# Performance work log

Hardware: AMD Instinct MI355X
Metric: run time of the kernel (lower is better)

Reference implementation:

```python
import jax, jax.numpy as jnp
import numpy as np

B, T, C, H = 8, 1024, 768, 12
D = C // H  # head_dim = 64

def _rope_tables(seq_len, d, base=10000.0):
    inv_freq = 1.0 / (base ** (jnp.arange(0, d, 2, dtype=jnp.float32) / d))  # [d/2]
    freqs = jnp.outer(jnp.arange(seq_len, dtype=jnp.float32), inv_freq)      # [T, d/2]
    return jnp.cos(freqs), jnp.sin(freqs)

def _apply_rotary(x, cos, sin):
    # x: [B,T,H,D]; cos/sin: [1,T,1,D/2]
    d = x.shape[-1] // 2
    x1, x2 = x[..., :d], x[..., d:]
    return jnp.concatenate([x1 * cos + x2 * sin, -x1 * sin + x2 * cos], axis=-1)

def setup_inputs() -> dict:
    key = jax.random.key(0)
    k1, k2, k3 = jax.random.split(key, 3)
    x = jax.random.normal(k1, (B, T, C), dtype=jnp.float32)
    w_qkv = jax.random.normal(k2, (3 * C, C), dtype=jnp.float32) * (C ** -0.5)
    w_proj = jax.random.normal(k3, (C, C), dtype=jnp.float32) * (C ** -0.5)
    return {"x": x, "w_qkv": w_qkv, "w_proj": w_proj}

def reference(x, w_qkv, w_proj):
    Bb, Tt, Cc = x.shape
    qkv = x @ w_qkv.T                                   # [B,T,3C]
    q, k, v = jnp.split(qkv, 3, axis=2)
    q = q.reshape(Bb, Tt, H, D)
    k = k.reshape(Bb, Tt, H, D)
    v = v.reshape(Bb, Tt, H, D)
    cos, sin = _rope_tables(Tt, D)
    cos = cos[None, :, None, :]
    sin = sin[None, :, None, :]
    q = _apply_rotary(q, cos, sin)
    k = _apply_rotary(k, cos, sin)
    scale = 1.0 / jnp.sqrt(jnp.float32(D))
    scores = jnp.einsum('bthd,bshd->bhts', q, k) * scale  # [B,H,T,T]
    causal = jnp.tril(jnp.ones((Tt, Tt), dtype=bool))
    scores = jnp.where(causal[None, None], scores, jnp.finfo(scores.dtype).min)
    p = jax.nn.softmax(scores, axis=-1)
    y = jnp.einsum('bhts,bshd->bthd', p, v).reshape(Bb, Tt, Cc)
    return y @ w_proj.T
```

## Files before the change

### kernel.cpp

```cpp
#include <hip/hip_runtime.h>
#include <hip/hip_bf16.h>

#define Bb 8
#define Tt 1024
#define Cc 768
#define Hh 12
#define Dd 64
#define M_ROWS (Bb * Tt)
#define QKV_N (3 * Cc)

typedef __attribute__((ext_vector_type(8))) short s16x8;
typedef __attribute__((ext_vector_type(4))) short s16x4;
typedef __attribute__((ext_vector_type(4))) float f32x4;

#define AS1 __attribute__((address_space(1)))
#define AS3 __attribute__((address_space(3)))

static __device__ __forceinline__ short f2bf(float f) {
    union { float f; unsigned u; } v; v.f = f;
    unsigned r = (v.u + 0x7fffu + ((v.u >> 16) & 1u)) >> 16;
    return (short)r;
}
static __device__ __forceinline__ unsigned pkt(float hi, float lo) {
    union { float f; unsigned u; } a, b; a.f = hi; b.f = lo;
    return __builtin_amdgcn_perm(a.u, b.u, 0x07060302u);
}

static __device__ __forceinline__ void cast8(const float* __restrict__ in,
                                             short* __restrict__ out, int i) {
    const float4 a = ((const float4*)in)[i * 2];
    const float4 b = ((const float4*)in)[i * 2 + 1];
    s16x8 f;
    f[0] = f2bf(a.x); f[1] = f2bf(a.y); f[2] = f2bf(a.z); f[3] = f2bf(a.w);
    f[4] = f2bf(b.x); f[5] = f2bf(b.y); f[6] = f2bf(b.z); f[7] = f2bf(b.w);
    ((s16x8*)out)[i] = f;
}

#define S1 (M_ROWS * Cc / 8)
#define S2 (QKV_N * Cc / 8)
#define S3 (Cc * Cc / 8)
#define SROPE (Tt * 32)
#define PREP_THREADS (S1 + S2 + S3 + SROPE)

__global__ __launch_bounds__(256) void prep_kernel(const float* __restrict__ x,
                                                   const float* __restrict__ wqkv,
                                                   const float* __restrict__ wproj,
                                                   short* __restrict__ xb,
                                                   short* __restrict__ wqkvb,
                                                   short* __restrict__ wprojb,
                                                   float2* __restrict__ cs) {
    int idx = blockIdx.x * blockDim.x + threadIdx.x;
    if (idx < S1) { cast8(x, xb, idx); return; }
    idx -= S1;
    if (idx < S2) {
        int row = idx / 96;
        int c8  = idx - row * 96;
        int q2 = (row >> 4) & 3;
        int src = (row < 2 * Cc && (q2 == 1 || q2 == 2)) ? (row ^ 0x30) : row;
        const float4 a = ((const float4*)(wqkv + (size_t)src * Cc))[c8 * 2];
        const float4 b = ((const float4*)(wqkv + (size_t)src * Cc))[c8 * 2 + 1];
        s16x8 f;
        f[0] = f2bf(a.x); f[1] = f2bf(a.y); f[2] = f2bf(a.z); f[3] = f2bf(a.w);
        f[4] = f2bf(b.x); f[5] = f2bf(b.y); f[6] = f2bf(b.z); f[7] = f2bf(b.w);
        ((s16x8*)wqkvb)[idx] = f;
        return;
    }
    idx -= S2;
    if (idx < S3) { cast8(wproj, wprojb, idx); return; }
    idx -= S3;
    {
        int t = idx >> 5, i = idx & 31;
        float inv_freq = exp2f(-0.41524101186092037f * (float)i);
        float fr = (float)t * inv_freq;
        float2 v; v.x = cosf(fr); v.y = sinf(fr);
        cs[idx] = v;
    }
}

template <int MODE, int TN>
__global__ __launch_bounds__(256, 3) void gemm_nt_mfma(const short* __restrict__ A,
                                                       const short* __restrict__ B,
                                                       void* __restrict__ Cout,
                                                       const float2* __restrict__ cs,
                                                       int M, int N, int K, int nblocks) {
    __shared__ short As[2][128 * 32];
    __shared__ short Bs[2][TN * 32];
    constexpr int NTW = TN / 32;

    const int wave = threadIdx.x >> 6;
    const int lane = threadIdx.x & 63;
    const int l16  = lane & 15;
    const int quad = lane >> 4;
    const int wr = wave >> 1;
    const int wc = wave & 1;

    const int mb8  = (M >> 7) >> 3;
    const int xcd  = blockIdx.x & 7;
    const int slot = blockIdx.x >> 3;
    const int bm = (xcd * mb8 + slot / nblocks) * 128;
    const int bn = (slot % nblocks) * TN;

    f32x4 acc[4][NTW] = {};

    auto stage = [&](int k0, int buf) {
#pragma unroll
        for (int j = 0; j < 2; j++) {
            const int D = j * 256 + wave * 64 + lane;
            const int G = D >> 3;
            const int s = (G << 3) | ((D & 7) ^ (G & 7));
            const int m = s >> 2, c4 = (s & 3) * 8;
            __builtin_amdgcn_global_load_lds(
                (const AS1 unsigned*)(A + (size_t)(bm + m) * K + k0 + c4),
                (AS3 unsigned*)&As[buf][(j * 256 + wave * 64) * 8], 16, 0, 0);
        }
        constexpr int BCH = TN * 4;
#pragma unroll
        for (int j = 0; j < (BCH + 255) / 256; j++) {
            if (BCH % 256 == 0 || j * 256 + wave * 64 < BCH) {
                const int D = j * 256 + wave * 64 + lane;
                const int G = D >> 3;
                const int s = (G << 3) | ((D & 7) ^ (G & 7));
                const int m = s >> 2, c4 = (s & 3) * 8;
                __builtin_amdgcn_global_load_lds(
                    (const AS1 unsigned*)(B + (size_t)(bn + m) * K + k0 + c4),
                    (AS3 unsigned*)&Bs[buf][(j * 256 + wave * 64) * 8], 16, 0, 0);
            }
        }
    };

    const int nIter = K >> 5;
    stage(0, 0);
    for (int kt = 0; kt < nIter; kt++) {
        const int buf = kt & 1;
        __syncthreads();
        if (kt + 1 < nIter) stage((kt + 1) << 5, buf ^ 1);

        s16x8 af[4];
#pragma unroll
        for (int mt = 0; mt < 4; mt++) {
            const int m = wr * 64 + mt * 16 + l16;
            const int d = ((m & 1) * 4 + quad) ^ ((m >> 1) & 7);
            af[mt] = *(const s16x8*)&As[buf][(m >> 1) * 64 + d * 8];
        }
#pragma unroll
        for (int nt = 0; nt < NTW; nt++) {
            const int n = wc * (TN / 2) + nt * 16 + l16;
            const int d = ((n & 1) * 4 + quad) ^ ((n >> 1) & 7);
            s16x8 bf = *(const s16x8*)&Bs[buf][(n >> 1) * 64 + d * 8];
#pragma unroll
            for (int mt = 0; mt < 4; mt++)
                acc[mt][nt] = __builtin_amdgcn_mfma_f32_16x16x32_bf16(
                    af[mt], bf, acc[mt][nt], 0, 0, 0);
        }
    }

    if constexpr (MODE == 0) {
#pragma unroll
        for (int mt = 0; mt < 4; mt++)
#pragma unroll
            for (int r = 0; r < 4; r++) {
                const size_t row = bm + wr * 64 + mt * 16 + quad * 4 + r;
#pragma unroll
                for (int nt = 0; nt < NTW; nt++)
                    ((float*)Cout)[row * N + bn + wc * (TN / 2) + nt * 16 + l16] =
                        acc[mt][nt][r];
            }
    } else {
        const bool is_v = (bn >= 2 * Cc);
        if (is_v) {
#pragma unroll
            for (int mt = 0; mt < 4; mt++)
#pragma unroll
                for (int r = 0; r < 4; r++) {
                    const size_t row = bm + wr * 64 + mt * 16 + quad * 4 + r;
#pragma unroll
                    for (int nt = 0; nt < NTW; nt++)
                        ((short*)Cout)[row * N + bn + wc * (TN / 2) + nt * 16 + l16] =
                            f2bf(acc[mt][nt][r]);
                }
        } else {
            const float scale = (bn < Cc) ? 0.125f : 1.0f;
#pragma unroll
            for (int mt = 0; mt < 4; mt++) {
#pragma unroll
                for (int r = 0; r < 4; r++) {
                    const int row = bm + wr * 64 + mt * 16 + quad * 4 + r;
                    const int t = row & (Tt - 1);
                    short* cp = (short*)Cout + (size_t)row * N + bn + wc * (TN / 2);
#pragma unroll
                    for (int p = 0; p < NTW; p += 2) {
                        const int g = wc * NTW + p;
                        const int i0 = ((g & 2) ? 16 : 0) + l16;
                        const float2 c0 = cs[t * 32 + i0];
                        const float x1 = acc[mt][p][r];
                        const float x2 = acc[mt][p + 1][r];
                        cp[p * 16 + l16]        = f2bf((x1 * c0.x + x2 * c0.y) * scale);
                        cp[(p + 1) * 16 + l16]  = f2bf((-x1 * c0.y + x2 * c0.x) * scale);
                    }
                }
            }
        }
    }
}

#define KSP 72
#define VSP 72

__global__ __launch_bounds__(256, 3) void flash_attn(const short* __restrict__ qkv,
                                                     short* __restrict__ y) {
    __shared__ short Ks[2][64 * KSP];
    __shared__ short Vs[2][64 * VSP];

    const int wave = threadIdx.x >> 6;
    const int lane = threadIdx.x & 63;
    const int l16  = lane & 15;
    const int quad = lane >> 4;

    const int pair = blockIdx.x / 96;
    const int bh   = blockIdx.x % 96;
    const int h = bh % Hh;
    const int b = bh / Hh;
    const int qa_blk = pair;
    const int qb_blk = 15 - pair;
    const int q0a = qa_blk * 64 + wave * 16;
    const int q0b = qb_blk * 64 + wave * 16;

    s16x8 qfa[2], qfb[2];
    {
        const short* qpa = qkv + (size_t)(b * Tt + q0a + l16) * QKV_N + h * Dd + quad * 8;
        const short* qpb = qkv + (size_t)(b * Tt + q0b + l16) * QKV_N + h * Dd + quad * 8;
        qfa[0] = *(const s16x8*)qpa;  qfa[1] = *(const s16x8*)(qpa + 32);
        qfb[0] = *(const s16x8*)qpb;  qfb[1] = *(const s16x8*)(qpb + 32);
    }

    f32x4 oa[4] = {}, ob[4] = {};
    float la = 0.f, lb = 0.f;

    const int krow = threadIdx.x >> 2;
    const int kd0  = (threadIdx.x & 3) * 16;
    const int key2 = (threadIdx.x & 31) * 2;
    const int dv0  = (threadIdx.x >> 5) * 8;

    s16x8 pk0, pk1, pv0, pv1;
    auto load_tile = [&](int kbase) {
        const short* kp = qkv + (size_t)(b * Tt + kbase + krow) * QKV_N + Cc + h * Dd + kd0;
        pk0 = *(const s16x8*)kp;
        pk1 = *(const s16x8*)(kp + 8);
        const short* vp = qkv + (size_t)(b * Tt + kbase + key2) * QKV_N + 2 * Cc + h * Dd + dv0;
        pv0 = *(const s16x8*)vp;
        pv1 = *(const s16x8*)(vp + QKV_N);
    };
    auto store_tile = [&](int buf) {
        *(s16x8*)&Ks[buf][krow * KSP + kd0]     = pk0;
        *(s16x8*)&Ks[buf][krow * KSP + kd0 + 8] = pk1;
#pragma unroll
        for (int j = 0; j < 8; j++) {
            ushort2 w; w.x = (unsigned short)pv0[j]; w.y = (unsigned short)pv1[j];
            *(ushort2*)&Vs[buf][(dv0 + j) * VSP + key2] = w;
        }
    };

    auto process_pair = [&](int buf, int kbase, bool mask_a) {
        short* pwb = &Ks[buf ^ 1][wave * 16 * KSP];
        short* pwa = &Vs[buf ^ 1][wave * 16 * VSP];
        f32x4 eb[4], ea[4];
#pragma unroll
        for (int g = 0; g < 4; g++) {
            s16x8 kf0 = *(const s16x8*)&Ks[buf][(g * 16 + l16) * KSP + quad * 8];
            s16x8 kf1 = *(const s16x8*)&Ks[buf][(g * 16 + l16) * KSP + 32 + quad * 8];
            f32x4 zb = {}, za = {};
            zb = __builtin_amdgcn_mfma_f32_16x16x32_bf16(kf0, qfb[0], zb, 0, 0, 0);
            zb = __builtin_amdgcn_mfma_f32_16x16x32_bf16(kf1, qfb[1], zb, 0, 0, 0);
            za = __builtin_amdgcn_mfma_f32_16x16x32_bf16(kf0, qfa[0], za, 0, 0, 0);
            za = __builtin_amdgcn_mfma_f32_16x16x32_bf16(kf1, qfa[1], za, 0, 0, 0);
            eb[g] = zb; ea[g] = za;
        }
        float rsb = 0.f, rsa = 0.f;
#pragma unroll
        for (int g = 0; g < 4; g++) {
#pragma unroll
            for (int r = 0; r < 4; r++) {
                float pb = __expf(eb[g][r]); rsb += pb; eb[g][r] = pb;
                float pa = __expf(ea[g][r]);
                if (mask_a) pa = (kbase + g * 16 + quad * 4 + r <= q0a + l16) ? pa : 0.0f;
                rsa += pa; ea[g][r] = pa;
            }
            uint2 ub, ua;
            ub.x = pkt(eb[g][1], eb[g][0]); ub.y = pkt(eb[g][3], eb[g][2]);
            ua.x = pkt(ea[g][1], ea[g][0]); ua.y = pkt(ea[g][3], ea[g][2]);
            *(uint2*)&pwb[l16 * KSP + g * 16 + quad * 4] = ub;
            *(uint2*)&pwa[l16 * VSP + g * 16 + quad * 4] = ua;
        }
        lb += rsb; la += rsa;
#pragma unroll
        for (int c = 0; c < 2; c++) {
            s16x8 pbb = *(const s16x8*)&pwb[l16 * KSP + c * 32 + quad * 8];
            s16x8 pba = *(const s16x8*)&pwa[l16 * VSP + c * 32 + quad * 8];
#pragma unroll
            for (int nc = 0; nc < 4; nc++) {
                s16x8 vb = *(const s16x8*)&Vs[buf][(nc * 16 + l16) * VSP + c * 32 + quad * 8];
                ob[nc] = __builtin_amdgcn_mfma_f32_16x16x32_bf16(vb, pbb, ob[nc], 0, 0, 0);
                oa[nc] = __builtin_amdgcn_mfma_f32_16x16x32_bf16(vb, pba, oa[nc], 0, 0, 0);
            }
        }
    };

    auto process_single = [&](int buf, int kbase, bool masked) {
        short* pw = &Ks[buf ^ 1][wave * 16 * KSP];
        f32x4 e[4];
#pragma unroll
        for (int g = 0; g < 4; g++) {
            s16x8 kf0 = *(const s16x8*)&Ks[buf][(g * 16 + l16) * KSP + quad * 8];
            s16x8 kf1 = *(const s16x8*)&Ks[buf][(g * 16 + l16) * KSP + 32 + quad * 8];
            f32x4 z = {};
            z = __builtin_amdgcn_mfma_f32_16x16x32_bf16(kf0, qfb[0], z, 0, 0, 0);
            z = __builtin_amdgcn_mfma_f32_16x16x32_bf16(kf1, qfb[1], z, 0, 0, 0);
            e[g] = z;
        }
        float rs = 0.f;
#pragma unroll
        for (int g = 0; g < 4; g++) {
#pragma unroll
            for (int r = 0; r < 4; r++) {
                float p = __expf(e[g][r]);
                if (masked) p = (kbase + g * 16 + quad * 4 + r <= q0b + l16) ? p : 0.0f;
                rs += p; e[g][r] = p;
            }
            uint2 u;
            u.x = pkt(e[g][1], e[g][0]); u.y = pkt(e[g][3], e[g][2]);
            *(uint2*)&pw[l16 * KSP + g * 16 + quad * 4] = u;
        }
        lb += rs;
#pragma unroll
        for (int c = 0; c < 2; c++) {
            s16x8 pb = *(const s16x8*)&pw[l16 * KSP + c * 32 + quad * 8];
#pragma unroll
            for (int nc = 0; nc < 4; nc++) {
                s16x8 vb = *(const s16x8*)&Vs[buf][(nc * 16 + l16) * VSP + c * 32 + quad * 8];
                ob[nc] = __builtin_amdgcn_mfma_f32_16x16x32_bf16(vb, pb, ob[nc], 0, 0, 0);
            }
        }
    };

    load_tile(0);
    store_tile(0);
    for (int kt = 0; kt <= qb_blk; kt++) {
        __syncthreads();
        const int nb = (kt < qb_blk) ? (kt + 1) * 64 : qb_blk * 64;
        load_tile(nb);
        const int buf = kt & 1;
        const int kbase = kt * 64;
        if (kt <= qa_blk)
            process_pair(buf, kbase, kt == qa_blk);
        else
            process_single(buf, kbase, kt == qb_blk);
        store_tile(buf ^ 1);
    }

    float sa = la; sa += __shfl_xor(sa, 16, 64); sa += __shfl_xor(sa, 32, 64);
    float sb = lb; sb += __shfl_xor(sb, 16, 64); sb += __shfl_xor(sb, 32, 64);
    const float inva = 1.0f / sa;
    const float invb = 1.0f / sb;
    short* ypa = y + (size_t)(b * Tt + q0a + l16) * Cc + h * Dd + quad * 4;
    short* ypb = y + (size_t)(b * Tt + q0b + l16) * Cc + h * Dd + quad * 4;
#pragma unroll
    for (int nc = 0; nc < 4; nc++) {
        s16x4 va, vb2;
#pragma unroll
        for (int r = 0; r < 4; r++) {
            va[r]  = f2bf(oa[nc][r] * inva);
            vb2[r] = f2bf(ob[nc][r] * invb);
        }
        *(s16x4*)&ypa[nc * 16] = va;
        *(s16x4*)&ypb[nc * 16] = vb2;
    }
}

extern "C" void kernel_launch(void* const* d_in, const int* in_sizes, int n_in,
                              void* d_out, int out_size, void* d_ws, size_t ws_size,
                              hipStream_t stream) {
    const float* x      = (const float*)d_in[0];
    const float* w_qkv  = (const float*)d_in[1];
    const float* w_proj = (const float*)d_in[2];
    float* out = (float*)d_out;

    float2* cs    = (float2*)d_ws;
    short* xb     = (short*)(cs + Tt * 32);
    short* wqkvb  = xb + (size_t)M_ROWS * Cc;
    short* wprojb = wqkvb + (size_t)QKV_N * Cc;
    short* qkvb   = wprojb + (size_t)Cc * Cc;
    short* yb     = qkvb + (size_t)M_ROWS * QKV_N;

    prep_kernel<<<PREP_THREADS / 256, 256, 0, stream>>>(
        x, w_qkv, w_proj, xb, wqkvb, wprojb, cs);

    gemm_nt_mfma<1, 192><<<768, 256, 0, stream>>>(
        xb, wqkvb, qkvb, cs, M_ROWS, QKV_N, Cc, QKV_N / 192);

    flash_attn<<<96 * 8, 256, 0, stream>>>(qkvb, yb);

    gemm_nt_mfma<0, 96><<<512, 256, 0, stream>>>(
        yb, wprojb, out, nullptr, M_ROWS, Cc, Cc, Cc / 96);
}
```

Baseline: 167.3 us.

## Replace QKV GEMM with 256x288-tile, 512-thread, 4-stage direct-to-LDS pipelined kernel

Adds a dedicated QKV projection kernel that uses large 256x288 tiles, 8 waves, and a 4-buffer LDS ring filled with global_load_lds, interleaving the next stages' loads with MFMA work and using s_setprio around MFMA bursts. Column blocks are mapped so each XCD handles a fixed N slice. Because the 288-wide tile splits a rotary pair across waves, one accumulator column is exchanged through LDS scratch in the epilogue. This aims to raise MFMA utilization and data reuse over the generic GEMM, at the cost of heavy register and LDS use and more complex epilogue logic.

```diff
diff --git a/kernel.cpp b/kernel.cpp
--- a/kernel.cpp
+++ b/kernel.cpp
@@ -203,6 +203,183 @@
     }
 }
 
+#define QBM 256
+#define QBN 288
+
+__global__ __launch_bounds__(512, 2) void qkv_gemm_8ph(const short* __restrict__ A,
+                                                       const short* __restrict__ Bw,
+                                                       short* __restrict__ Cq,
+                                                       const float2* __restrict__ cs) {
+    __shared__ short As[4][QBM * 32];
+    __shared__ short Bs[4][QBN * 32];
+
+    const int tid  = threadIdx.x;
+    const int wave = tid >> 6;
+    const int lane = tid & 63;
+    const int l16  = lane & 15;
+    const int quad = lane >> 4;
+    const int wr   = wave >> 1;
+    const int wc   = wave & 1;
+
+    const int xcd = blockIdx.x & 7;
+    const int bn  = xcd * QBN;
+    const int bm  = (blockIdx.x >> 3) * QBM;
+    const int gt0 = xcd * 18;
+
+    int aoff0, boff0, boffR;
+    {
+        const int G = tid >> 3;
+        const int s = (G << 3) | ((tid & 7) ^ (G & 7));
+        aoff0 = (s >> 2) * Cc + (s & 3) * 8;
+        boff0 = aoff0;
+    }
+    {
+        const int D = 1024 + (wave & 1) * 64 + lane;
+        const int G = D >> 3;
+        const int s = (G << 3) | ((D & 7) ^ (G & 7));
+        boffR = (s >> 2) * Cc + (s & 3) * 8;
+    }
+    const short* Ag = A + (size_t)bm * Cc;
+    const short* Bg = Bw + (size_t)bn * Cc;
+
+    const int mA = wr * 64 + l16;
+    const int abase = (mA >> 1) * 128 + ((((mA & 1) * 4 + quad) ^ ((mA >> 1) & 7)) * 16);
+    const int nB = wc * 144 + l16;
+    const int bbase = (nB >> 1) * 128 + ((((nB & 1) * 4 + quad) ^ ((nB >> 1) & 7)) * 16);
+
+    f32x4 acc[4][9] = {};
+
+#define STG_A(J, SB, K0) __builtin_amdgcn_global_load_lds(                    \
+        (const AS1 unsigned*)(Ag + aoff0 + (J) * (128 * Cc) + (K0)),          \
+        (AS3 unsigned*)&As[SB][((J) * 512 + wave * 64) * 8], 16, 0, 0)
+#define STG_B(J, SB, K0) __builtin_amdgcn_global_load_lds(                    \
+        (const AS1 unsigned*)(Bg + boff0 + (J) * (128 * Cc) + (K0)),          \
+        (AS3 unsigned*)&Bs[SB][((J) * 512 + wave * 64) * 8], 16, 0, 0)
+#define STG_BR(SB, K0) __builtin_amdgcn_global_load_lds(                      \
+        (const AS1 unsigned*)(Bg + boffR + (K0)),                             \
+        (AS3 unsigned*)&Bs[SB][(1024 + (wave & 1) * 64) * 8], 16, 0, 0)
+
+#pragma unroll
+    for (int t = 0; t < 3; t++) {
+        const int k0 = t << 5;
+        STG_A(0, t, k0); STG_A(1, t, k0);
+        STG_B(0, t, k0); STG_B(1, t, k0); STG_BR(t, k0);
+    }
+    asm volatile("s_waitcnt vmcnt(10)" ::: "memory");
+    __builtin_amdgcn_s_barrier();
+    asm volatile("" ::: "memory");
+
+    for (int kt = 0; kt < 24; kt++) {
+        const int buf  = kt & 3;
+        const int sb   = (kt + 3) & 3;
+        const int k0n  = (kt + 3) << 5;
+        const bool st  = (kt < 21);
+        const char* ap = (const char*)&As[buf][0];
+        const char* bp = (const char*)&Bs[buf][0];
+
+        if (st) { STG_A(0, sb, k0n); STG_A(1, sb, k0n); STG_B(0, sb, k0n); }
+        s16x8 bf[9];
+#pragma unroll
+        for (int nt = 0; nt < 9; nt++)
+            bf[nt] = *(const s16x8*)(bp + bbase + nt * 1024);
+        {
+            s16x8 a0 = *(const s16x8*)(ap + abase);
+            s16x8 a1 = *(const s16x8*)(ap + abase + 1024);
+            __builtin_amdgcn_s_setprio(1);
+#pragma unroll
+            for (int nt = 0; nt < 9; nt++) {
+                acc[0][nt] = __builtin_amdgcn_mfma_f32_16x16x32_bf16(a0, bf[nt], acc[0][nt], 0, 0, 0);
+                acc[1][nt] = __builtin_amdgcn_mfma_f32_16x16x32_bf16(a1, bf[nt], acc[1][nt], 0, 0, 0);
+            }
+            __builtin_amdgcn_s_setprio(0);
+        }
+        if (st) { STG_B(1, sb, k0n); STG_BR(sb, k0n); }
+        {
+            s16x8 a2 = *(const s16x8*)(ap + abase + 2048);
+            s16x8 a3 = *(const s16x8*)(ap + abase + 3072);
+            __builtin_amdgcn_s_setprio(1);
+#pragma unroll
+            for (int nt = 0; nt < 9; nt++) {
+                acc[2][nt] = __builtin_amdgcn_mfma_f32_16x16x32_bf16(a2, bf[nt], acc[2][nt], 0, 0, 0);
+                acc[3][nt] = __builtin_amdgcn_mfma_f32_16x16x32_bf16(a3, bf[nt], acc[3][nt], 0, 0, 0);
+            }
+            __builtin_amdgcn_s_setprio(0);
+        }
+        if (kt < 23) {
+            if (kt < 21)       asm volatile("s_waitcnt vmcnt(10)" ::: "memory");
+            else if (kt == 21) asm volatile("s_waitcnt vmcnt(5)"  ::: "memory");
+            else               asm volatile("s_waitcnt vmcnt(0)"  ::: "memory");
+            __builtin_amdgcn_s_barrier();
+            asm volatile("" ::: "memory");
+        }
+    }
+
+    __builtin_amdgcn_s_barrier();
+    asm volatile("" ::: "memory");
+    float* scr = (float*)&As[0][0];
+    const int po = wc ? 0 : 8;
+#pragma unroll
+    for (int mt = 0; mt < 4; mt++)
+#pragma unroll
+        for (int r = 0; r < 4; r++)
+            scr[(((wc * 4 + wr) * 4 + mt) * 16 + quad * 4 + r) * 16 + l16] =
+                acc[mt][po][r];
+    __builtin_amdgcn_s_barrier();
+    asm volatile("" ::: "memory");
+
+#pragma unroll
+    for (int mt = 0; mt < 4; mt++) {
+#pragma unroll
+        for (int r = 0; r < 4; r++) {
+            const int row = bm + wr * 64 + mt * 16 + quad * 4 + r;
+            const int t = row & (Tt - 1);
+            short* cp = Cq + (size_t)row * QKV_N + bn + wc * 144;
+#pragma unroll
+            for (int pp = 0; pp < 4; pp++) {
+                const int p = wc + 2 * pp;
+                const int g = gt0 + wc * 9 + p;
+                const float x1 = acc[mt][p][r];
+                const float x2 = acc[mt][p + 1][r];
+                if (g < 96) {
+                    const int i0 = ((g & 2) ? 16 : 0) + l16;
+                    const float2 c0 = cs[t * 32 + i0];
+                    const float sc = (g < 48) ? 0.125f : 1.0f;
+                    cp[p * 16 + l16]       = f2bf((x1 * c0.x + x2 * c0.y) * sc);
+                    cp[(p + 1) * 16 + l16] = f2bf((-x1 * c0.y + x2 * c0.x) * sc);
+                } else {
+                    cp[p * 16 + l16]       = f2bf(x1);
+                    cp[(p + 1) * 16 + l16] = f2bf(x2);
+                }
+            }
+            const float xo = acc[mt][po][r];
+            const float xp = scr[((((wc ^ 1) * 4 + wr) * 4 + mt) * 16 + quad * 4 + r) * 16 + l16];
+            const int ge = gt0 + 8;
+            if (wc == 0) {
+                if (ge < 96) {
+                    const int i0 = ((ge & 2) ? 16 : 0) + l16;
+                    const float2 c0 = cs[t * 32 + i0];
+                    const float sc = (ge < 48) ? 0.125f : 1.0f;
+                    cp[8 * 16 + l16] = f2bf((xo * c0.x + xp * c0.y) * sc);
+                } else {
+                    cp[8 * 16 + l16] = f2bf(xo);
+                }
+            } else {
+                if (ge < 96) {
+                    const int i0 = ((ge & 2) ? 16 : 0) + l16;
+                    const float2 c0 = cs[t * 32 + i0];
+                    const float sc = (ge < 48) ? 0.125f : 1.0f;
+                    cp[l16] = f2bf((-xp * c0.y + xo * c0.x) * sc);
+                } else {
+                    cp[l16] = f2bf(xo);
+                }
+            }
+        }
+    }
+#undef STG_A
+#undef STG_B
+#undef STG_BR
+}
+
 #define KSP 72
 #define VSP 72
 
@@ -394,8 +571,7 @@
     prep_kernel<<<PREP_THREADS / 256, 256, 0, stream>>>(
         x, w_qkv, w_proj, xb, wqkvb, wprojb, cs);
 
-    gemm_nt_mfma<1, 192><<<768, 256, 0, stream>>>(
-        xb, wqkvb, qkvb, cs, M_ROWS, QKV_N, Cc, QKV_N / 192);
+    qkv_gemm_8ph<<<256, 512, 0, stream>>>(xb, wqkvb, qkvb, cs);
 
     flash_attn<<<96 * 8, 256, 0, stream>>>(qkvb, yb);
 
```

New measurement: 221.9 us. 32.6% more time.
